# Performance work log

Measured on AMD Instinct MI355X. Metric: run time of the kernel, lower is better.

Reference implementation:

```python
import jax, jax.numpy as jnp
import numpy as np

BS, S, DM, H = 4, 512, 512, 8
DK = DM // H
EPS = 1e-6


def setup_inputs() -> dict:
    key = jax.random.key(0)
    ks = jax.random.split(key, 11)
    sc = jnp.float32(0.02)  # small init so exp(q @ k^T) stays finite (no max-subtraction in original)
    return {
        "q": jax.random.normal(ks[0], (BS, S, DM), jnp.float32),
        "k": jax.random.normal(ks[1], (BS, S, DM), jnp.float32),
        "v": jax.random.normal(ks[2], (BS, S, DM), jnp.float32),
        "Wq": sc * jax.random.normal(ks[3], (DM, DM), jnp.float32),
        "bq": jnp.zeros((DM,), jnp.float32),
        "Wk": sc * jax.random.normal(ks[4], (DM, DM), jnp.float32),
        "bk": jnp.zeros((DM,), jnp.float32),
        "Wv": sc * jax.random.normal(ks[5], (DM, DM), jnp.float32),
        "bv": jnp.zeros((DM,), jnp.float32),
        "Wo": sc * jax.random.normal(ks[6], (DM, DM), jnp.float32),
        "bo": jnp.zeros((DM,), jnp.float32),
        "alpha": jnp.ones((DK,), jnp.float32),   # Norm.alpha over last dim (= d_k per head)
        "beta": jnp.zeros((DK,), jnp.float32),   # Norm.bias
    }


def reference(q, k, v, Wq, bq, Wk, bk, Wv, bv, Wo, bo, alpha, beta):
    # project and split heads: [bs, h, s, d_k]
    qh = (q @ Wq + bq).reshape(BS, S, H, DK).transpose(0, 2, 1, 3)
    kh = (k @ Wk + bk).reshape(BS, S, H, DK).transpose(0, 2, 1, 3)
    vh = (v @ Wv + bv).reshape(BS, S, H, DK).transpose(0, 2, 1, 3)

    # pairwise-batch exp scores: E[bq, bk, h, i, j] = exp(q[bq] @ k[bk]^T)
    E = jnp.exp(jnp.einsum('bhid,chjd->bchij', qh, kh))  # [BS, BS, H, S, S]
    # fenmu: sum over k-batch, each term scaled by sqrt(d_k) (as in original loop)
    fenmu = jnp.sqrt(jnp.float32(DK)) * E.sum(axis=1)     # [BS, H, S, S]
    # fenzi: same-batch exp scores (diagonal of pairwise tensor)
    fenzi = E[jnp.arange(BS), jnp.arange(BS)]             # [BS, H, S, S]
    R = fenzi / fenmu                                     # [BS, H, S, S]

    # per v-batch-entry score: score[bq, c] = R[bq] @ v[c]
    score = jnp.einsum('bhij,chjd->bchid', R, vh)         # [BS, BS, H, S, DK]
    sm = jax.nn.softmax(score, axis=-1)
    # Norm: torch.std is unbiased (ddof=1); eps added to std, not variance
    mu = sm.mean(axis=-1, keepdims=True)
    std = jnp.sqrt(sm.var(axis=-1, ddof=1, keepdims=True))
    ln = alpha * (sm - mu) / (std + EPS) + beta

    # output += LN(score) + q, accumulated over the v-batch loop (BS iterations)
    heads = ln.sum(axis=1) + jnp.float32(BS) * qh         # [BS, H, S, DK]
    concat = heads.transpose(0, 2, 1, 3).reshape(BS, S, DM)
    return concat @ Wo + bo
```

## Files before the change

kernel.cpp:

```cpp
#include <hip/hip_runtime.h>
#include <hip/hip_bf16.h>

#define BSZ 4
#define SEQ 512
#define DMODEL 512
#define NHEAD 8
#define DKH 64
#define EPSLN 1e-6f

typedef short bf16x8 __attribute__((ext_vector_type(8)));
typedef float f32x4 __attribute__((ext_vector_type(4)));

static __device__ __forceinline__ short f2bf(float x) {
  unsigned u = __builtin_bit_cast(unsigned, x);
  u = (u + 0x7FFFu + ((u >> 16) & 1u)) >> 16;
  return (short)u;
}
static __device__ __forceinline__ bf16x8 cvt8(float4 a, float4 b) {
  bf16x8 r;
  r[0] = f2bf(a.x); r[1] = f2bf(a.y); r[2] = f2bf(a.z); r[3] = f2bf(a.w);
  r[4] = f2bf(b.x); r[5] = f2bf(b.y); r[6] = f2bf(b.z); r[7] = f2bf(b.w);
  return r;
}
static __device__ __forceinline__ unsigned pk2(float a, float b) {
  return (unsigned)(unsigned short)f2bf(a) |
         ((unsigned)(unsigned short)f2bf(b) << 16);
}
static __device__ __forceinline__ void async_cp16(const void* g, void* l) {
  __builtin_amdgcn_global_load_lds(
      (const __attribute__((address_space(1))) unsigned int*)g,
      (__attribute__((address_space(3))) unsigned int*)l, 16, 0, 0);
}

__global__ __launch_bounds__(256) void prep_kernel(
    const float* __restrict__ q, const float* __restrict__ k,
    const float* __restrict__ v, short* __restrict__ qb,
    short* __restrict__ kb, short* __restrict__ vb,
    const float* __restrict__ Wq, const float* __restrict__ Wk,
    const float* __restrict__ Wv, const float* __restrict__ Wo,
    short* __restrict__ Wqt, short* __restrict__ Wkt,
    short* __restrict__ Wvt, short* __restrict__ Wot) {
  __shared__ float T[64][65];
  const int bx = blockIdx.x;
  if (bx < 1536) {
    const int which = bx >> 9, blk = bx & 511;
    const float* s; short* d;
    switch (which) {
      case 0: s = q; d = qb; break;
      case 1: s = k; d = kb; break;
      default: s = v; d = vb; break;
    }
    const size_t idx = (size_t)blk * 2048 + (size_t)threadIdx.x * 8;
    float4 a = *(const float4*)&s[idx];
    float4 b = *(const float4*)&s[idx + 4];
    *(bf16x8*)&d[idx] = cvt8(a, b);
    return;
  }
  const int r = bx - 1536;
  const int mat = r >> 6, m = r & 63;
  const int k0 = (m & 7) * 64, n0 = (m >> 3) * 64;
  const float* src; short* dst;
  switch (mat) {
    case 0: src = Wq; dst = Wqt; break;
    case 1: src = Wk; dst = Wkt; break;
    case 2: src = Wv; dst = Wvt; break;
    default: src = Wo; dst = Wot; break;
  }
  const int tid = threadIdx.x;
  const int n4 = (tid & 15) * 4, kk = tid >> 4;
#pragma unroll
  for (int p = 0; p < 4; ++p) {
    float4 w4 = *(const float4*)&src[(size_t)(k0 + kk + p * 16) * DMODEL + n0 + n4];
    T[kk + p * 16][n4 + 0] = w4.x;
    T[kk + p * 16][n4 + 1] = w4.y;
    T[kk + p * 16][n4 + 2] = w4.z;
    T[kk + p * 16][n4 + 3] = w4.w;
  }
  __syncthreads();
  const int k4 = (tid & 15) * 4;
#pragma unroll
  for (int p = 0; p < 4; ++p) {
    const int nn = (tid >> 4) + p * 16;
    float x0 = T[k4 + 0][nn], x1 = T[k4 + 1][nn];
    float x2 = T[k4 + 2][nn], x3 = T[k4 + 3][nn];
    uint2 u; u.x = pk2(x0, x1); u.y = pk2(x2, x3);
    *(uint2*)&dst[(size_t)(n0 + nn) * DMODEL + k0 + k4] = u;
  }
}

__device__ __forceinline__ void gemm_body(
    const short* __restrict__ A, const short* __restrict__ Wt,
    const float* __restrict__ bias, void* __restrict__ out, int omode) {
  __shared__ short As[2][128 * 32];
  __shared__ short Bs[2][128 * 32];
  const int tid = threadIdx.x;
  const int w = tid >> 6, lane = tid & 63;
  const int l15 = lane & 15, q = lane >> 4;
  const int wm = w >> 1, wn = w & 1;
  const int bn = blockIdx.x * 128, bm = blockIdx.y * 128;
  const int wu = __builtin_amdgcn_readfirstlane(w);
  const int srow = wu * 16 + (lane >> 2);
  const int sch = lane & 3;

  f32x4 acc[4][4] = {};

#define GSTAGE(k0, buf)                                                      \
  {                                                                          \
    const short* ga0 = A + (size_t)(bm + srow) * 512 + (k0) + sch * 8;       \
    const short* ga1 = A + (size_t)(bm + srow + 64) * 512 + (k0) + sch * 8;  \
    const short* gb0 = Wt + (size_t)(bn + srow) * 512 + (k0) + sch * 8;      \
    const short* gb1 = Wt + (size_t)(bn + srow + 64) * 512 + (k0) + sch * 8; \
    async_cp16(ga0, &As[buf][wu * 512]);                                     \
    async_cp16(ga1, &As[buf][(4 + wu) * 512]);                               \
    async_cp16(gb0, &Bs[buf][wu * 512]);                                     \
    async_cp16(gb1, &Bs[buf][(4 + wu) * 512]);                               \
  }

  GSTAGE(0, 0);
  for (int ks = 0; ks < 16; ++ks) {
    __syncthreads();
    if (ks < 15) GSTAGE((ks + 1) * 32, (ks + 1) & 1);
    const short* a = As[ks & 1];
    const short* bsh = Bs[ks & 1];
    bf16x8 af[4], bfr[4];
#pragma unroll
    for (int mt = 0; mt < 4; ++mt)
      af[mt] = *(const bf16x8*)&a[(wm * 64 + mt * 16 + l15) * 32 + q * 8];
#pragma unroll
    for (int nt = 0; nt < 4; ++nt)
      bfr[nt] = *(const bf16x8*)&bsh[(wn * 64 + nt * 16 + l15) * 32 + q * 8];
#pragma unroll
    for (int mt = 0; mt < 4; ++mt)
#pragma unroll
      for (int nt = 0; nt < 4; ++nt)
        acc[mt][nt] = __builtin_amdgcn_mfma_f32_16x16x32_bf16(
            af[mt], bfr[nt], acc[mt][nt], 0, 0, 0);
  }
#undef GSTAGE

  float bv[4];
#pragma unroll
  for (int nt = 0; nt < 4; ++nt) bv[nt] = bias[bn + wn * 64 + nt * 16 + l15];
#pragma unroll
  for (int mt = 0; mt < 4; ++mt)
#pragma unroll
    for (int nt = 0; nt < 4; ++nt) {
      const int col = bn + wn * 64 + nt * 16 + l15;
#pragma unroll
      for (int r = 0; r < 4; ++r) {
        const int row = bm + wm * 64 + mt * 16 + q * 4 + r;
        const float val = acc[mt][nt][r] + bv[nt];
        if (omode == 0) {
          ((float*)out)[(size_t)row * 512 + col] = val;
        } else if (omode == 1) {
          ((short*)out)[(size_t)row * 512 + col] = f2bf(val);
        } else {
          const int cc = row >> 9, j = row & 511;
          const int hh = col >> 6, d = col & 63;
          ((short*)out)[(((size_t)(cc * 8 + hh) * 64 + d) << 9) + j] = f2bf(val);
        }
      }
    }
}

__global__ __launch_bounds__(256, 2) void proj_gemm(
    const short* qb, const short* kb, const short* vb,
    const short* Wqt, const short* Wkt, const short* Wvt,
    const float* bq, const float* bk, const float* bvs,
    float* Qp, short* Kb, short* Vt) {
  const short* A; const short* Wt; const float* bias; void* out; int omode;
  switch (blockIdx.z) {
    case 0: A = qb; Wt = Wqt; bias = bq; out = Qp; omode = 0; break;
    case 1: A = kb; Wt = Wkt; bias = bk; out = Kb; omode = 1; break;
    default: A = vb; Wt = Wvt; bias = bvs; out = Vt; omode = 2; break;
  }
  gemm_body(A, Wt, bias, out, omode);
}

__global__ __launch_bounds__(256, 2) void out_gemm(
    const short* Hc, const short* Wot, const float* bo, float* out) {
  gemm_body(Hc, Wot, bo, out, 0);
}

__global__ __launch_bounds__(256, 3) void attn2_kernel(
    const float* __restrict__ Qp, const short* __restrict__ Kb,
    const short* __restrict__ Vt, const float* __restrict__ alpha,
    const float* __restrict__ beta, short* __restrict__ Hc) {
  __shared__ __align__(16) short Stage[2][2 * 4096];
  __shared__ __align__(16) short Rs[32][72];
  __shared__ __align__(16) float xch[16 * 128];

  const int bx = blockIdx.x;
  const int h = bx & 7;
  const int b = (bx >> 3) & 3;
  const int it = bx >> 5;
  const int i0 = it * 32;
  const int tid = threadIdx.x;
  const int w = tid >> 6, lane = tid & 63;
  const int l15 = lane & 15, q = lane >> 4;
  const int wi = w >> 1, wj = w & 1;
  const int wu = __builtin_amdgcn_readfirstlane(w);

  const float* qrow =
      Qp + (size_t)(b * SEQ + i0 + wi * 16 + l15) * DMODEL + h * DKH;
  const bf16x8 aq0 = cvt8(*(const float4*)(qrow + q * 8),
                          *(const float4*)(qrow + q * 8 + 4));
  const bf16x8 aq1 = cvt8(*(const float4*)(qrow + 32 + q * 8),
                          *(const float4*)(qrow + 32 + q * 8 + 4));

  const int srow0 = wu * 8 + (lane >> 3);
  const int scol = (lane & 7) ^ (lane >> 3);

  const short* kbase_h = Kb + h * DKH;
  const short* vbase_h = Vt + (((size_t)h * DKH) << 9);

#define STG1(g0, rs, buf, tslot)                                          \
  {                                                                       \
    async_cp16((g0) + (size_t)srow0 * (rs) + scol * 8,                    \
               &Stage[buf][(tslot) * 4096 + wu * 512]);                   \
    async_cp16((g0) + (size_t)(srow0 + 32) * (rs) + scol * 8,             \
               &Stage[buf][(tslot) * 4096 + (4 + wu) * 512]);             \
  }
#define KTILE(c, j0) (kbase_h + ((size_t)((c) * SEQ) + (j0)) * DMODEL)
#define VTILE(c, j0) (vbase_h + (((size_t)((c) * NHEAD * DKH)) << 9) + (j0))

  f32x4 acc[4][4] = {};
  float sacc[2][4], ebb[2][4];

  STG1(KTILE(0, 0), DMODEL, 0, 0);
  STG1(KTILE(1, 0), DMODEL, 0, 1);

  for (int jt = 0; jt < 8; ++jt) {
    const int j0 = jt * 64;
    bf16x8 ar;
#pragma unroll
    for (int ph2 = 0; ph2 < 4; ++ph2) {
      __syncthreads();
      const int buf = ph2 & 1, nbuf = buf ^ 1;
      if (ph2 == 0) {
        STG1(KTILE(2, j0), DMODEL, nbuf, 0);
        STG1(KTILE(3, j0), DMODEL, nbuf, 1);
      } else if (ph2 == 1) {
        STG1(VTILE(0, j0), SEQ, nbuf, 0);
        STG1(VTILE(1, j0), SEQ, nbuf, 1);
      } else if (ph2 == 2) {
        STG1(VTILE(2, j0), SEQ, nbuf, 0);
        STG1(VTILE(3, j0), SEQ, nbuf, 1);
      } else if (jt < 7) {
        STG1(KTILE(0, j0 + 64), DMODEL, nbuf, 0);
        STG1(KTILE(1, j0 + 64), DMODEL, nbuf, 1);
      }
      if (ph2 < 2) {
        if (ph2 == 0) {
#pragma unroll
          for (int t = 0; t < 2; ++t)
#pragma unroll
            for (int r = 0; r < 4; ++r) { sacc[t][r] = 0.0f; ebb[t][r] = 0.0f; }
        }
#pragma unroll
        for (int ct = 0; ct < 2; ++ct) {
          const int c = ph2 * 2 + ct;
          const short* S = &Stage[buf][ct * 4096];
#pragma unroll
          for (int ntl = 0; ntl < 2; ++ntl) {
            const int row = (wj * 2 + ntl) * 16 + l15;
            const int p0 = q ^ (l15 & 7);
            bf16x8 b0 = *(const bf16x8*)&S[row * 64 + p0 * 8];
            bf16x8 b1 = *(const bf16x8*)&S[row * 64 + (p0 ^ 4) * 8];
            f32x4 s = {};
            s = __builtin_amdgcn_mfma_f32_16x16x32_bf16(aq0, b0, s, 0, 0, 0);
            s = __builtin_amdgcn_mfma_f32_16x16x32_bf16(aq1, b1, s, 0, 0, 0);
#pragma unroll
            for (int r = 0; r < 4; ++r) {
              const float e = __expf(s[r]);
              sacc[ntl][r] += e;
              ebb[ntl][r] = (c == b) ? e : ebb[ntl][r];
            }
          }
        }
        if (ph2 == 1) {
#pragma unroll
          for (int ntl = 0; ntl < 2; ++ntl)
#pragma unroll
            for (int r = 0; r < 4; ++r)
              Rs[wi * 16 + q * 4 + r][(wj * 2 + ntl) * 16 + l15] =
                  f2bf(ebb[ntl][r] / (8.0f * sacc[ntl][r]));
        }
      } else {
        if (ph2 == 2) ar = *(const bf16x8*)&Rs[wi * 16 + l15][wj * 32 + q * 8];
#pragma unroll
        for (int ct = 0; ct < 2; ++ct) {
          const int c = (ph2 - 2) * 2 + ct;
          const short* S = &Stage[buf][ct * 4096];
#pragma unroll
          for (int nt = 0; nt < 4; ++nt) {
            const int row = nt * 16 + l15;
            const int pb = (wj * 4 + q) ^ (l15 & 7);
            bf16x8 bv = *(const bf16x8*)&S[row * 64 + pb * 8];
            acc[c][nt] = __builtin_amdgcn_mfma_f32_16x16x32_bf16(
                ar, bv, acc[c][nt], 0, 0, 0);
          }
        }
      }
    }
  }
#undef STG1
#undef KTILE
#undef VTILE

#pragma unroll
  for (int c = 0; c < BSZ; ++c) {
    if (wj == 1) {
#pragma unroll
      for (int nt = 0; nt < 4; ++nt)
#pragma unroll
        for (int r = 0; r < 4; ++r)
          xch[(nt * 4 + r) * 128 + wi * 64 + lane] = acc[c][nt][r];
    }
    __syncthreads();
    if (wj == 0) {
#pragma unroll
      for (int nt = 0; nt < 4; ++nt)
#pragma unroll
        for (int r = 0; r < 4; ++r)
          acc[c][nt][r] += xch[(nt * 4 + r) * 128 + wi * 64 + lane];
    }
    __syncthreads();
  }

  if (wj == 0) {
    float al[4], be[4];
#pragma unroll
    for (int nt = 0; nt < 4; ++nt) {
      al[nt] = alpha[nt * 16 + l15];
      be[nt] = beta[nt * 16 + l15];
    }
    float hacc[4][4] = {};
#pragma unroll
    for (int c = 0; c < BSZ; ++c) {
#pragma unroll
      for (int r = 0; r < 4; ++r) {
        float e0 = __expf(acc[c][0][r]), e1 = __expf(acc[c][1][r]);
        float e2 = __expf(acc[c][2][r]), e3 = __expf(acc[c][3][r]);
        float es = e0 + e1 + e2 + e3;
#pragma unroll
        for (int m = 8; m >= 1; m >>= 1) es += __shfl_xor(es, m);
        const float inv = 1.0f / es;
        const float d0 = e0 * inv - 0.015625f, d1 = e1 * inv - 0.015625f;
        const float d2 = e2 * inv - 0.015625f, d3 = e3 * inv - 0.015625f;
        float sq = d0 * d0 + d1 * d1 + d2 * d2 + d3 * d3;
#pragma unroll
        for (int m = 8; m >= 1; m >>= 1) sq += __shfl_xor(sq, m);
        const float rs = 1.0f / (sqrtf(sq * (1.0f / 63.0f)) + EPSLN);
        hacc[r][0] += al[0] * d0 * rs + be[0];
        hacc[r][1] += al[1] * d1 * rs + be[1];
        hacc[r][2] += al[2] * d2 * rs + be[2];
        hacc[r][3] += al[3] * d3 * rs + be[3];
      }
    }
#pragma unroll
    for (int r = 0; r < 4; ++r) {
      const size_t rowoff =
          (size_t)(b * SEQ + i0 + wi * 16 + q * 4 + r) * DMODEL + h * DKH;
#pragma unroll
      for (int nt = 0; nt < 4; ++nt) {
        const int d = nt * 16 + l15;
        const float o = hacc[r][nt] + 4.0f * Qp[rowoff + d];
        Hc[rowoff + d] = f2bf(o);
      }
    }
  }
}

extern "C" void kernel_launch(void* const* d_in, const int* in_sizes, int n_in,
                              void* d_out, int out_size, void* d_ws,
                              size_t ws_size, hipStream_t stream) {
  (void)in_sizes; (void)n_in; (void)out_size; (void)ws_size;
  const float* q = (const float*)d_in[0];
  const float* k = (const float*)d_in[1];
  const float* v = (const float*)d_in[2];
  const float* Wq = (const float*)d_in[3];
  const float* bq = (const float*)d_in[4];
  const float* Wk = (const float*)d_in[5];
  const float* bk = (const float*)d_in[6];
  const float* Wv = (const float*)d_in[7];
  const float* bv = (const float*)d_in[8];
  const float* Wo = (const float*)d_in[9];
  const float* bo = (const float*)d_in[10];
  const float* alpha = (const float*)d_in[11];
  const float* beta = (const float*)d_in[12];
  float* out = (float*)d_out;

  char* wsb = (char*)d_ws;
  short* qb = (short*)(wsb);
  short* kb = (short*)(wsb + (2u << 20));
  short* vb = (short*)(wsb + (4u << 20));
  float* Qp = (float*)(wsb + (6u << 20));
  short* Kb = (short*)(wsb + (10u << 20));
  short* Vtg = (short*)(wsb + (12u << 20));
  short* Hc = (short*)(wsb + (14u << 20));
  short* Wqt = (short*)(wsb + (16u << 20));
  short* Wkt = (short*)(wsb + (16u << 20) + (512u << 10));
  short* Wvt = (short*)(wsb + (17u << 20));
  short* Wot = (short*)(wsb + (17u << 20) + (512u << 10));

  prep_kernel<<<dim3(1792), 256, 0, stream>>>(q, k, v, qb, kb, vb,
                                              Wq, Wk, Wv, Wo,
                                              Wqt, Wkt, Wvt, Wot);
  proj_gemm<<<dim3(4, 16, 3), 256, 0, stream>>>(qb, kb, vb, Wqt, Wkt, Wvt,
                                                bq, bk, bv, Qp, Kb, Vtg);
  attn2_kernel<<<dim3(512), 256, 0, stream>>>(Qp, Kb, Vtg, alpha, beta, Hc);
  out_gemm<<<dim3(4, 16), 256, 0, stream>>>(Hc, Wot, bo, out);
}
```

Measured before the change: 149.6 us.

## Give each wave 16 full query rows, doubling block tile to 64 rows

Result: slower. 154.8 us (+3.4%).

```diff
diff --git a/kernel.cpp b/kernel.cpp
--- a/kernel.cpp
+++ b/kernel.cpp
@@ -182,27 +182,25 @@
   gemm_body(Hc, Wot, bo, out, 0);
 }
 
-__global__ __launch_bounds__(256, 3) void attn2_kernel(
+__global__ __launch_bounds__(256, 1) void attn3_kernel(
     const float* __restrict__ Qp, const short* __restrict__ Kb,
     const short* __restrict__ Vt, const float* __restrict__ alpha,
     const float* __restrict__ beta, short* __restrict__ Hc) {
   __shared__ __align__(16) short Stage[2][2 * 4096];
-  __shared__ __align__(16) short Rs[32][72];
-  __shared__ __align__(16) float xch[16 * 128];
+  __shared__ __align__(16) short Rs[64][72];
 
   const int bx = blockIdx.x;
   const int h = bx & 7;
   const int b = (bx >> 3) & 3;
   const int it = bx >> 5;
-  const int i0 = it * 32;
+  const int i0 = it * 64;
   const int tid = threadIdx.x;
   const int w = tid >> 6, lane = tid & 63;
   const int l15 = lane & 15, q = lane >> 4;
-  const int wi = w >> 1, wj = w & 1;
   const int wu = __builtin_amdgcn_readfirstlane(w);
 
   const float* qrow =
-      Qp + (size_t)(b * SEQ + i0 + wi * 16 + l15) * DMODEL + h * DKH;
+      Qp + (size_t)(b * SEQ + i0 + w * 16 + l15) * DMODEL + h * DKH;
   const bf16x8 aq0 = cvt8(*(const float4*)(qrow + q * 8),
                           *(const float4*)(qrow + q * 8 + 4));
   const bf16x8 aq1 = cvt8(*(const float4*)(qrow + 32 + q * 8),
@@ -225,14 +223,14 @@
 #define VTILE(c, j0) (vbase_h + (((size_t)((c) * NHEAD * DKH)) << 9) + (j0))
 
   f32x4 acc[4][4] = {};
-  float sacc[2][4], ebb[2][4];
+  float sacc[4][4], ebb[4][4];
 
   STG1(KTILE(0, 0), DMODEL, 0, 0);
   STG1(KTILE(1, 0), DMODEL, 0, 1);
 
   for (int jt = 0; jt < 8; ++jt) {
     const int j0 = jt * 64;
-    bf16x8 ar;
+    bf16x8 ar0, ar1;
 #pragma unroll
     for (int ph2 = 0; ph2 < 4; ++ph2) {
       __syncthreads();
@@ -253,7 +251,7 @@
       if (ph2 < 2) {
         if (ph2 == 0) {
 #pragma unroll
-          for (int t = 0; t < 2; ++t)
+          for (int t = 0; t < 4; ++t)
 #pragma unroll
             for (int r = 0; r < 4; ++r) { sacc[t][r] = 0.0f; ebb[t][r] = 0.0f; }
         }
@@ -262,8 +260,8 @@
           const int c = ph2 * 2 + ct;
           const short* S = &Stage[buf][ct * 4096];
 #pragma unroll
-          for (int ntl = 0; ntl < 2; ++ntl) {
-            const int row = (wj * 2 + ntl) * 16 + l15;
+          for (int ntl = 0; ntl < 4; ++ntl) {
+            const int row = ntl * 16 + l15;
             const int p0 = q ^ (l15 & 7);
             bf16x8 b0 = *(const bf16x8*)&S[row * 64 + p0 * 8];
             bf16x8 b1 = *(const bf16x8*)&S[row * 64 + (p0 ^ 4) * 8];
@@ -280,14 +278,17 @@
         }
         if (ph2 == 1) {
 #pragma unroll
-          for (int ntl = 0; ntl < 2; ++ntl)
+          for (int ntl = 0; ntl < 4; ++ntl)
 #pragma unroll
             for (int r = 0; r < 4; ++r)
-              Rs[wi * 16 + q * 4 + r][(wj * 2 + ntl) * 16 + l15] =
+              Rs[w * 16 + q * 4 + r][ntl * 16 + l15] =
                   f2bf(ebb[ntl][r] / (8.0f * sacc[ntl][r]));
         }
       } else {
-        if (ph2 == 2) ar = *(const bf16x8*)&Rs[wi * 16 + l15][wj * 32 + q * 8];
+        if (ph2 == 2) {
+          ar0 = *(const bf16x8*)&Rs[w * 16 + l15][q * 8];
+          ar1 = *(const bf16x8*)&Rs[w * 16 + l15][32 + q * 8];
+        }
 #pragma unroll
         for (int ct = 0; ct < 2; ++ct) {
           const int c = (ph2 - 2) * 2 + ct;
@@ -295,10 +296,13 @@
 #pragma unroll
           for (int nt = 0; nt < 4; ++nt) {
             const int row = nt * 16 + l15;
-            const int pb = (wj * 4 + q) ^ (l15 & 7);
-            bf16x8 bv = *(const bf16x8*)&S[row * 64 + pb * 8];
+            const int p0 = q ^ (l15 & 7);
+            bf16x8 bv0 = *(const bf16x8*)&S[row * 64 + p0 * 8];
+            bf16x8 bv1 = *(const bf16x8*)&S[row * 64 + (p0 ^ 4) * 8];
             acc[c][nt] = __builtin_amdgcn_mfma_f32_16x16x32_bf16(
-                ar, bv, acc[c][nt], 0, 0, 0);
+                ar0, bv0, acc[c][nt], 0, 0, 0);
+            acc[c][nt] = __builtin_amdgcn_mfma_f32_16x16x32_bf16(
+                ar1, bv1, acc[c][nt], 0, 0, 0);
           }
         }
       }
@@ -308,66 +312,44 @@
 #undef KTILE
 #undef VTILE
 
+  float al[4], be[4];
+#pragma unroll
+  for (int nt = 0; nt < 4; ++nt) {
+    al[nt] = alpha[nt * 16 + l15];
+    be[nt] = beta[nt * 16 + l15];
+  }
+  float hacc[4][4] = {};
 #pragma unroll
   for (int c = 0; c < BSZ; ++c) {
-    if (wj == 1) {
-#pragma unroll
-      for (int nt = 0; nt < 4; ++nt)
-#pragma unroll
-        for (int r = 0; r < 4; ++r)
-          xch[(nt * 4 + r) * 128 + wi * 64 + lane] = acc[c][nt][r];
-    }
-    __syncthreads();
-    if (wj == 0) {
-#pragma unroll
-      for (int nt = 0; nt < 4; ++nt)
-#pragma unroll
-        for (int r = 0; r < 4; ++r)
-          acc[c][nt][r] += xch[(nt * 4 + r) * 128 + wi * 64 + lane];
-    }
-    __syncthreads();
-  }
-
-  if (wj == 0) {
-    float al[4], be[4];
+#pragma unroll
+    for (int r = 0; r < 4; ++r) {
+      float e0 = __expf(acc[c][0][r]), e1 = __expf(acc[c][1][r]);
+      float e2 = __expf(acc[c][2][r]), e3 = __expf(acc[c][3][r]);
+      float es = e0 + e1 + e2 + e3;
+#pragma unroll
+      for (int m = 8; m >= 1; m >>= 1) es += __shfl_xor(es, m);
+      const float inv = 1.0f / es;
+      const float d0 = e0 * inv - 0.015625f, d1 = e1 * inv - 0.015625f;
+      const float d2 = e2 * inv - 0.015625f, d3 = e3 * inv - 0.015625f;
+      float sq = d0 * d0 + d1 * d1 + d2 * d2 + d3 * d3;
+#pragma unroll
+      for (int m = 8; m >= 1; m >>= 1) sq += __shfl_xor(sq, m);
+      const float rs = 1.0f / (sqrtf(sq * (1.0f / 63.0f)) + EPSLN);
+      hacc[r][0] += al[0] * d0 * rs + be[0];
+      hacc[r][1] += al[1] * d1 * rs + be[1];
+      hacc[r][2] += al[2] * d2 * rs + be[2];
+      hacc[r][3] += al[3] * d3 * rs + be[3];
+    }
+  }
+#pragma unroll
+  for (int r = 0; r < 4; ++r) {
+    const size_t rowoff =
+        (size_t)(b * SEQ + i0 + w * 16 + q * 4 + r) * DMODEL + h * DKH;
 #pragma unroll
     for (int nt = 0; nt < 4; ++nt) {
-      al[nt] = alpha[nt * 16 + l15];
-      be[nt] = beta[nt * 16 + l15];
-    }
-    float hacc[4][4] = {};
-#pragma unroll
-    for (int c = 0; c < BSZ; ++c) {
-#pragma unroll
-      for (int r = 0; r < 4; ++r) {
-        float e0 = __expf(acc[c][0][r]), e1 = __expf(acc[c][1][r]);
-        float e2 = __expf(acc[c][2][r]), e3 = __expf(acc[c][3][r]);
-        float es = e0 + e1 + e2 + e3;
-#pragma unroll
-        for (int m = 8; m >= 1; m >>= 1) es += __shfl_xor(es, m);
-        const float inv = 1.0f / es;
-        const float d0 = e0 * inv - 0.015625f, d1 = e1 * inv - 0.015625f;
-        const float d2 = e2 * inv - 0.015625f, d3 = e3 * inv - 0.015625f;
-        float sq = d0 * d0 + d1 * d1 + d2 * d2 + d3 * d3;
-#pragma unroll
-        for (int m = 8; m >= 1; m >>= 1) sq += __shfl_xor(sq, m);
-        const float rs = 1.0f / (sqrtf(sq * (1.0f / 63.0f)) + EPSLN);
-        hacc[r][0] += al[0] * d0 * rs + be[0];
-        hacc[r][1] += al[1] * d1 * rs + be[1];
-        hacc[r][2] += al[2] * d2 * rs + be[2];
-        hacc[r][3] += al[3] * d3 * rs + be[3];
-      }
-    }
-#pragma unroll
-    for (int r = 0; r < 4; ++r) {
-      const size_t rowoff =
-          (size_t)(b * SEQ + i0 + wi * 16 + q * 4 + r) * DMODEL + h * DKH;
-#pragma unroll
-      for (int nt = 0; nt < 4; ++nt) {
-        const int d = nt * 16 + l15;
-        const float o = hacc[r][nt] + 4.0f * Qp[rowoff + d];
-        Hc[rowoff + d] = f2bf(o);
-      }
+      const int d = nt * 16 + l15;
+      const float o = hacc[r][nt] + 4.0f * Qp[rowoff + d];
+      Hc[rowoff + d] = f2bf(o);
     }
   }
 }
@@ -409,6 +391,6 @@
                                               Wqt, Wkt, Wvt, Wot);
   proj_gemm<<<dim3(4, 16, 3), 256, 0, stream>>>(qb, kb, vb, Wqt, Wkt, Wvt,
                                                 bq, bk, bv, Qp, Kb, Vtg);
-  attn2_kernel<<<dim3(512), 256, 0, stream>>>(Qp, Kb, Vtg, alpha, beta, Hc);
+  attn3_kernel<<<dim3(256), 256, 0, stream>>>(Qp, Kb, Vtg, alpha, beta, Hc);
   out_gemm<<<dim3(4, 16), 256, 0, stream>>>(Hc, Wot, bo, out);
 }
```
